# Kernel tuning notes

Hardware: AMD Instinct MI355X
Metric: run time of the kernel (lower is better)

The kernel has to match this reference:

```python
import jax, jax.numpy as jnp
import numpy as np

N, C_IN, C_OUT, H, RANK = 16, 4, 32, 400, 4


def setup_inputs() -> dict:
    key = jax.random.key(0)
    k1, k2, k3 = jax.random.split(key, 3)
    x = jax.random.normal(k1, (N, C_IN, H, H), dtype=jnp.float32)
    # symmetric sylo: weight_R tied to weight_L (shape C_out x C_in x H x rank)
    fan_in = C_IN * H
    scale = 1.0 / np.sqrt(fan_in)
    weight_L = jax.random.normal(k2, (C_OUT, C_IN, H, RANK), dtype=jnp.float32) * scale
    bias = jax.random.uniform(k3, (C_OUT,), dtype=jnp.float32, minval=-scale, maxval=scale)
    return {"x": x, "weight_L": weight_L, "bias": bias}


def reference(x, weight_L, bias):
    # Expand low-rank symmetric template: T[o,c] = L[o,c] @ L[o,c].T  (H x H)
    T = jnp.einsum('ocir,ocjr->ocij', weight_L, weight_L)
    # Crosshair similarity, summed over input channels:
    # out[n,o,i,j] = sum_c [ sum_k X[n,c,i,k]T[o,c,i,k] + sum_k X[n,c,k,j]T[o,c,k,j] - X[n,c,i,j]T[o,c,i,j] ]
    rows = jnp.einsum('ncik,ocik->noi', x, T)   # row sums of X*T
    cols = jnp.einsum('nckj,ockj->noj', x, T)   # column sums of X*T
    diag = jnp.einsum('ncij,ocij->noij', x, T)  # pointwise term (counted twice)
    out = rows[..., :, None] + cols[..., None, :] - diag
    return out + bias[None, :, None, None]
```

## Files before the change

kernel.cpp:

```cpp
#include <hip/hip_runtime.h>

#define H  400
#define NB 16
#define CI 4
#define CO 32

#define TT 80
__global__ __launch_bounds__(256) void k_transpose(const float* __restrict__ x,
                                                   float* __restrict__ xt) {
    __shared__ float tile[TT][TT + 5];
    int b = blockIdx.x;
    int tj = b % 5;
    int ti = (b / 5) % 5;
    int nc = b / 25;
    const float* src = x + (size_t)nc * H * H;
    float* dst = xt + (size_t)nc * H * H;
    int i0 = ti * TT, j0 = tj * TT;
    for (int e = threadIdx.x; e < TT * 20; e += 256) {
        int r = e / 20, q = e % 20;
        float4 v = ((const float4*)(src + (size_t)(i0 + r) * H + j0))[q];
        tile[r][q * 4 + 0] = v.x; tile[r][q * 4 + 1] = v.y;
        tile[r][q * 4 + 2] = v.z; tile[r][q * 4 + 3] = v.w;
    }
    __syncthreads();
    for (int e = threadIdx.x; e < TT * 20; e += 256) {
        int r = e / 20, q = e % 20;
        float4 v;
        v.x = tile[q * 4 + 0][r]; v.y = tile[q * 4 + 1][r];
        v.z = tile[q * 4 + 2][r]; v.w = tile[q * 4 + 3][r];
        ((float4*)(dst + (size_t)(j0 + r) * H + i0))[q] = v;
    }
}

#define KC 40
#define KSPLIT 5
__global__ __launch_bounds__(256) void k_rowscols(const float* __restrict__ x,
        const float* __restrict__ xt, const float* __restrict__ L,
        float* __restrict__ rowsP, float* __restrict__ colsP)
{
    __shared__ __align__(16) float4 Lm[CO * CI];
    __shared__ __align__(16) float Xr[NB * CI * KC];
    __shared__ __align__(16) float Xc[NB * CI * KC];
    __shared__ __align__(16) float Tr[CO * 164];
    int b = blockIdx.x;
    int m  = b / KSPLIT;
    int ks = b % KSPLIT;
    int tid = threadIdx.x;
    const float4* L4 = (const float4*)L;
    if (tid < CO * CI) Lm[tid] = L4[tid * H + m];

    int o  = tid & 31;
    int n0 = tid >> 5;
    int n1 = n0 + 8;
    float ar0 = 0.f, ar1 = 0.f, ac0 = 0.f, ac1 = 0.f;

    for (int ch = 0; ch < 2; ++ch) {
        int k0 = ks * 80 + ch * KC;
        __syncthreads();
        for (int e = tid; e < NB * CI * KC / 4; e += 256) {
            int q  = e % 10;
            int nc = e / 10;
            ((float4*)Xr)[e] = *(const float4*)(x  + (size_t)(nc * H + m) * H + k0 + q * 4);
            ((float4*)Xc)[e] = *(const float4*)(xt + (size_t)(nc * H + m) * H + k0 + q * 4);
        }
        for (int e = tid; e < CO * CI * KC; e += 256) {
            int k  = e % KC;
            int oc = e / KC;
            float4 lv = L4[oc * H + k0 + k];
            float4 lm = Lm[oc];
            Tr[(oc >> 2) * 164 + (oc & 3) * KC + k] =
                lv.x * lm.x + lv.y * lm.y + lv.z * lm.z + lv.w * lm.w;
        }
        __syncthreads();
        #pragma unroll
        for (int c = 0; c < CI; ++c) {
            const float4* trp = (const float4*)(Tr + o * 164 + c * KC);
            const float4* pr0 = (const float4*)(Xr + (n0 * CI + c) * KC);
            const float4* pr1 = (const float4*)(Xr + (n1 * CI + c) * KC);
            const float4* pc0 = (const float4*)(Xc + (n0 * CI + c) * KC);
            const float4* pc1 = (const float4*)(Xc + (n1 * CI + c) * KC);
            #pragma unroll
            for (int q = 0; q < KC / 4; ++q) {
                float4 tv = trp[q];
                float4 a  = pr0[q];
                float4 bb = pr1[q];
                float4 cc = pc0[q];
                float4 dd = pc1[q];
                ar0 += tv.x * a.x  + tv.y * a.y  + tv.z * a.z  + tv.w * a.w;
                ar1 += tv.x * bb.x + tv.y * bb.y + tv.z * bb.z + tv.w * bb.w;
                ac0 += tv.x * cc.x + tv.y * cc.y + tv.z * cc.z + tv.w * cc.w;
                ac1 += tv.x * dd.x + tv.y * dd.y + tv.z * dd.z + tv.w * dd.w;
            }
        }
    }
    size_t base = (size_t)ks * NB * CO * H;
    rowsP[base + (size_t)(n0 * CO + o) * H + m] = ar0;
    rowsP[base + (size_t)(n1 * CO + o) * H + m] = ar1;
    colsP[base + (size_t)(n0 * CO + o) * H + m] = ac0;
    colsP[base + (size_t)(n1 * CO + o) * H + m] = ac1;
}

__global__ __launch_bounds__(256) void k_reduce(const float* __restrict__ rowsP,
        const float* __restrict__ colsP, float* __restrict__ rows, float* __restrict__ cols)
{
    int i = blockIdx.x * 256 + threadIdx.x;
    if (i < NB * CO * H) {
        float s = 0.f, t = 0.f;
        #pragma unroll
        for (int k = 0; k < KSPLIT; ++k) {
            s += rowsP[(size_t)k * NB * CO * H + i];
            t += colsP[(size_t)k * NB * CO * H + i];
        }
        rows[i] = s;
        cols[i] = t;
    }
}

#define TS 16
__global__ __launch_bounds__(512) void k_out(const float* __restrict__ x,
        const float* __restrict__ L, const float* __restrict__ bias,
        const float* __restrict__ rows, const float* __restrict__ cols,
        float* __restrict__ out)
{
    __shared__ __align__(16) float Xl[NB * CI * TS * TS];
    __shared__ __align__(16) float rT[NB * 8 * TS];
    __shared__ __align__(16) float cT[NB * 8 * TS];
    int b = blockIdx.x;
    int ti = b / 25, tj = b % 25;
    int i0 = ti * TS, j0 = tj * TS;
    int tid = threadIdx.x;

    const float4* x4 = (const float4*)x;
    float4* Xl4 = (float4*)Xl;
    for (int e = tid; e < NB * CI * TS * 4; e += 512) {
        int q  = e & 3;
        int ii = (e >> 2) & 15;
        int nc = e >> 6;
        Xl4[e] = x4[(size_t)(nc * H + i0 + ii) * 100 + tj * 4 + q];
    }

    int o  = tid >> 6;
    int u  = tid & 63;
    int ii = u >> 2, jq = u & 3;
    const float4* L4 = (const float4*)L;
    const float4* cT4 = (const float4*)cT;
    float4* out4 = (float4*)out;

    for (int os = 0; os < 4; ++os) {
        int og = os * 8 + o;
        float4 T4[CI];
        #pragma unroll
        for (int c = 0; c < CI; ++c) {
            float4 Li = L4[(og * CI + c) * H + i0 + ii];
            float4 La = L4[(og * CI + c) * H + j0 + jq * 4 + 0];
            float4 Lb = L4[(og * CI + c) * H + j0 + jq * 4 + 1];
            float4 Lc = L4[(og * CI + c) * H + j0 + jq * 4 + 2];
            float4 Ld = L4[(og * CI + c) * H + j0 + jq * 4 + 3];
            T4[c].x = Li.x * La.x + Li.y * La.y + Li.z * La.z + Li.w * La.w;
            T4[c].y = Li.x * Lb.x + Li.y * Lb.y + Li.z * Lb.z + Li.w * Lb.w;
            T4[c].z = Li.x * Lc.x + Li.y * Lc.y + Li.z * Lc.z + Li.w * Lc.w;
            T4[c].w = Li.x * Ld.x + Li.y * Ld.y + Li.z * Ld.z + Li.w * Ld.w;
        }
        float bo = bias[og];

        __syncthreads();
        for (int e = tid; e < NB * 8 * TS; e += 512) {
            int iw = e & 15;
            int oo = (e >> 4) & 7;
            int n  = e >> 7;
            rT[e] = rows[(size_t)(n * CO + os * 8 + oo) * H + i0 + iw];
            cT[e] = cols[(size_t)(n * CO + os * 8 + oo) * H + j0 + iw];
        }
        __syncthreads();

        for (int n = 0; n < NB; ++n) {
            float ra = rT[(n * 8 + o) * TS + ii] + bo;
            float4 ca = cT4[(n * 8 + o) * 4 + jq];
            float4 acc;
            acc.x = ra + ca.x; acc.y = ra + ca.y; acc.z = ra + ca.z; acc.w = ra + ca.w;
            #pragma unroll
            for (int c = 0; c < CI; ++c) {
                float4 xv = Xl4[((n * CI + c) * TS + ii) * 4 + jq];
                acc.x -= xv.x * T4[c].x;
                acc.y -= xv.y * T4[c].y;
                acc.z -= xv.z * T4[c].z;
                acc.w -= xv.w * T4[c].w;
            }
            out4[((size_t)(n * CO + og) * H + i0 + ii) * 100 + tj * 4 + jq] = acc;
        }
    }
}

extern "C" void kernel_launch(void* const* d_in, const int* in_sizes, int n_in,
                              void* d_out, int out_size, void* d_ws, size_t ws_size,
                              hipStream_t stream) {
    const float* x    = (const float*)d_in[0];
    const float* L    = (const float*)d_in[1];
    const float* bias = (const float*)d_in[2];
    float* out = (float*)d_out;
    char* ws = (char*)d_ws;

    size_t xt_bytes = (size_t)NB * CI * H * H * sizeof(float);
    size_t rc_elems = (size_t)NB * CO * H;
    size_t rcP_bytes = (size_t)KSPLIT * rc_elems * sizeof(float);
    size_t rc_bytes  = rc_elems * sizeof(float);

    float* XT    = (float*)ws;
    float* rowsP = (float*)(ws + xt_bytes);
    float* colsP = (float*)(ws + xt_bytes + rcP_bytes);
    float* rows  = (float*)(ws + xt_bytes + 2 * rcP_bytes);
    float* cols  = (float*)(ws + xt_bytes + 2 * rcP_bytes + rc_bytes);
    (void)ws_size;

    k_transpose<<<1600, 256, 0, stream>>>(x, XT);
    k_rowscols<<<H * KSPLIT, 256, 0, stream>>>(x, XT, L, rowsP, colsP);
    k_reduce<<<(NB * CO * H + 255) / 256, 256, 0, stream>>>(rowsP, colsP, rows, cols);
    k_out<<<625, 512, 0, stream>>>(x, L, bias, rows, cols, out);
}
```

Measured before the change: 508.4 us.

## Shrink k_out blocks to 256 threads, split batch in halves; coalesce partial writes

k_out now runs 256-thread blocks that process the batch in two halves of 8 and loop over 8 output-channel groups of 4. This cuts shared memory per block so more blocks can be resident per CU, which should help latency hiding. k_rowscols now writes partial sums in an (ks, m, n*o) layout so each block's stores are contiguous, and k_reduce reads that layout and transposes back. In exchange, T is recomputed from L twice as often in k_out, there are more barriers, and k_reduce's reads become strided.

```diff
diff --git a/kernel.cpp b/kernel.cpp
--- a/kernel.cpp
+++ b/kernel.cpp
@@ -51,7 +51,6 @@
 
     int o  = tid & 31;
     int n0 = tid >> 5;
-    int n1 = n0 + 8;
     float ar0 = 0.f, ar1 = 0.f, ac0 = 0.f, ac1 = 0.f;
 
     for (int ch = 0; ch < 2; ++ch) {
@@ -76,9 +75,9 @@
         for (int c = 0; c < CI; ++c) {
             const float4* trp = (const float4*)(Tr + o * 164 + c * KC);
             const float4* pr0 = (const float4*)(Xr + (n0 * CI + c) * KC);
-            const float4* pr1 = (const float4*)(Xr + (n1 * CI + c) * KC);
+            const float4* pr1 = (const float4*)(Xr + ((n0 + 8) * CI + c) * KC);
             const float4* pc0 = (const float4*)(Xc + (n0 * CI + c) * KC);
-            const float4* pc1 = (const float4*)(Xc + (n1 * CI + c) * KC);
+            const float4* pc1 = (const float4*)(Xc + ((n0 + 8) * CI + c) * KC);
             #pragma unroll
             for (int q = 0; q < KC / 4; ++q) {
                 float4 tv = trp[q];
@@ -93,100 +92,104 @@
             }
         }
     }
-    size_t base = (size_t)ks * NB * CO * H;
-    rowsP[base + (size_t)(n0 * CO + o) * H + m] = ar0;
-    rowsP[base + (size_t)(n1 * CO + o) * H + m] = ar1;
-    colsP[base + (size_t)(n0 * CO + o) * H + m] = ac0;
-    colsP[base + (size_t)(n1 * CO + o) * H + m] = ac1;
+    size_t base = ((size_t)ks * H + m) * (NB * CO);
+    rowsP[base + tid]       = ar0;
+    rowsP[base + 256 + tid] = ar1;
+    colsP[base + tid]       = ac0;
+    colsP[base + 256 + tid] = ac1;
 }
 
 __global__ __launch_bounds__(256) void k_reduce(const float* __restrict__ rowsP,
         const float* __restrict__ colsP, float* __restrict__ rows, float* __restrict__ cols)
 {
     int i = blockIdx.x * 256 + threadIdx.x;
-    if (i < NB * CO * H) {
-        float s = 0.f, t = 0.f;
-        #pragma unroll
-        for (int k = 0; k < KSPLIT; ++k) {
-            s += rowsP[(size_t)k * NB * CO * H + i];
-            t += colsP[(size_t)k * NB * CO * H + i];
-        }
-        rows[i] = s;
-        cols[i] = t;
-    }
+    int m  = i % H;
+    int no = i / H;
+    float s = 0.f, t = 0.f;
+    #pragma unroll
+    for (int k = 0; k < KSPLIT; ++k) {
+        s += rowsP[((size_t)k * H + m) * (NB * CO) + no];
+        t += colsP[((size_t)k * H + m) * (NB * CO) + no];
+    }
+    rows[(size_t)no * H + m] = s;
+    cols[(size_t)no * H + m] = t;
 }
 
 #define TS 16
-__global__ __launch_bounds__(512) void k_out(const float* __restrict__ x,
+__global__ __launch_bounds__(256, 4) void k_out(const float* __restrict__ x,
         const float* __restrict__ L, const float* __restrict__ bias,
         const float* __restrict__ rows, const float* __restrict__ cols,
         float* __restrict__ out)
 {
-    __shared__ __align__(16) float Xl[NB * CI * TS * TS];
-    __shared__ __align__(16) float rT[NB * 8 * TS];
-    __shared__ __align__(16) float cT[NB * 8 * TS];
+    __shared__ __align__(16) float Xl[8 * CI * TS * TS];
+    __shared__ __align__(16) float rT[8 * 4 * TS];
+    __shared__ __align__(16) float cT[8 * 4 * TS];
     int b = blockIdx.x;
     int ti = b / 25, tj = b % 25;
     int i0 = ti * TS, j0 = tj * TS;
     int tid = threadIdx.x;
 
-    const float4* x4 = (const float4*)x;
-    float4* Xl4 = (float4*)Xl;
-    for (int e = tid; e < NB * CI * TS * 4; e += 512) {
-        int q  = e & 3;
-        int ii = (e >> 2) & 15;
-        int nc = e >> 6;
-        Xl4[e] = x4[(size_t)(nc * H + i0 + ii) * 100 + tj * 4 + q];
-    }
-
     int o  = tid >> 6;
     int u  = tid & 63;
     int ii = u >> 2, jq = u & 3;
-    const float4* L4 = (const float4*)L;
+    const float4* x4  = (const float4*)x;
+    const float4* L4  = (const float4*)L;
     const float4* cT4 = (const float4*)cT;
+    float4* Xl4  = (float4*)Xl;
     float4* out4 = (float4*)out;
 
-    for (int os = 0; os < 4; ++os) {
-        int og = os * 8 + o;
-        float4 T4[CI];
-        #pragma unroll
-        for (int c = 0; c < CI; ++c) {
-            float4 Li = L4[(og * CI + c) * H + i0 + ii];
-            float4 La = L4[(og * CI + c) * H + j0 + jq * 4 + 0];
-            float4 Lb = L4[(og * CI + c) * H + j0 + jq * 4 + 1];
-            float4 Lc = L4[(og * CI + c) * H + j0 + jq * 4 + 2];
-            float4 Ld = L4[(og * CI + c) * H + j0 + jq * 4 + 3];
-            T4[c].x = Li.x * La.x + Li.y * La.y + Li.z * La.z + Li.w * La.w;
-            T4[c].y = Li.x * Lb.x + Li.y * Lb.y + Li.z * Lb.z + Li.w * Lb.w;
-            T4[c].z = Li.x * Lc.x + Li.y * Lc.y + Li.z * Lc.z + Li.w * Lc.w;
-            T4[c].w = Li.x * Ld.x + Li.y * Ld.y + Li.z * Ld.z + Li.w * Ld.w;
-        }
-        float bo = bias[og];
-
-        __syncthreads();
-        for (int e = tid; e < NB * 8 * TS; e += 512) {
-            int iw = e & 15;
-            int oo = (e >> 4) & 7;
-            int n  = e >> 7;
-            rT[e] = rows[(size_t)(n * CO + os * 8 + oo) * H + i0 + iw];
-            cT[e] = cols[(size_t)(n * CO + os * 8 + oo) * H + j0 + iw];
-        }
-        __syncthreads();
-
-        for (int n = 0; n < NB; ++n) {
-            float ra = rT[(n * 8 + o) * TS + ii] + bo;
-            float4 ca = cT4[(n * 8 + o) * 4 + jq];
-            float4 acc;
-            acc.x = ra + ca.x; acc.y = ra + ca.y; acc.z = ra + ca.z; acc.w = ra + ca.w;
+    for (int nh = 0; nh < 2; ++nh) {
+        if (nh) __syncthreads();
+        for (int e = tid; e < 8 * CI * TS * 4; e += 256) {
+            int q   = e & 3;
+            int iiw = (e >> 2) & 15;
+            int nc  = nh * (8 * CI) + (e >> 6);
+            Xl4[e] = x4[(size_t)(nc * H + i0 + iiw) * 100 + tj * 4 + q];
+        }
+        for (int os = 0; os < 8; ++os) {
+            int og = os * 4 + o;
+            float4 T4[CI];
             #pragma unroll
             for (int c = 0; c < CI; ++c) {
-                float4 xv = Xl4[((n * CI + c) * TS + ii) * 4 + jq];
-                acc.x -= xv.x * T4[c].x;
-                acc.y -= xv.y * T4[c].y;
-                acc.z -= xv.z * T4[c].z;
-                acc.w -= xv.w * T4[c].w;
-            }
-            out4[((size_t)(n * CO + og) * H + i0 + ii) * 100 + tj * 4 + jq] = acc;
+                float4 Li = L4[(og * CI + c) * H + i0 + ii];
+                float4 La = L4[(og * CI + c) * H + j0 + jq * 4 + 0];
+                float4 Lb = L4[(og * CI + c) * H + j0 + jq * 4 + 1];
+                float4 Lc = L4[(og * CI + c) * H + j0 + jq * 4 + 2];
+                float4 Ld = L4[(og * CI + c) * H + j0 + jq * 4 + 3];
+                T4[c].x = Li.x * La.x + Li.y * La.y + Li.z * La.z + Li.w * La.w;
+                T4[c].y = Li.x * Lb.x + Li.y * Lb.y + Li.z * Lb.z + Li.w * Lb.w;
+                T4[c].z = Li.x * Lc.x + Li.y * Lc.y + Li.z * Lc.z + Li.w * Lc.w;
+                T4[c].w = Li.x * Ld.x + Li.y * Ld.y + Li.z * Ld.z + Li.w * Ld.w;
+            }
+            float bo = bias[og];
+
+            __syncthreads();
+            for (int e = tid; e < 8 * 4 * TS; e += 256) {
+                int iw = e & 15;
+                int oo = (e >> 4) & 3;
+                int np = e >> 6;
+                int n  = nh * 8 + np;
+                rT[e] = rows[(size_t)(n * CO + os * 4 + oo) * H + i0 + iw];
+                cT[e] = cols[(size_t)(n * CO + os * 4 + oo) * H + j0 + iw];
+            }
+            __syncthreads();
+
+            for (int np = 0; np < 8; ++np) {
+                float ra  = rT[(np * 4 + o) * TS + ii] + bo;
+                float4 ca = cT4[(np * 4 + o) * 4 + jq];
+                float4 acc;
+                acc.x = ra + ca.x; acc.y = ra + ca.y; acc.z = ra + ca.z; acc.w = ra + ca.w;
+                #pragma unroll
+                for (int c = 0; c < CI; ++c) {
+                    float4 xv = Xl4[((np * CI + c) * TS + ii) * 4 + jq];
+                    acc.x -= xv.x * T4[c].x;
+                    acc.y -= xv.y * T4[c].y;
+                    acc.z -= xv.z * T4[c].z;
+                    acc.w -= xv.w * T4[c].w;
+                }
+                int n = nh * 8 + np;
+                out4[((size_t)(n * CO + og) * H + i0 + ii) * 100 + tj * 4 + jq] = acc;
+            }
         }
     }
 }
@@ -214,6 +217,6 @@
 
     k_transpose<<<1600, 256, 0, stream>>>(x, XT);
     k_rowscols<<<H * KSPLIT, 256, 0, stream>>>(x, XT, L, rowsP, colsP);
-    k_reduce<<<(NB * CO * H + 255) / 256, 256, 0, stream>>>(rowsP, colsP, rows, cols);
-    k_out<<<625, 512, 0, stream>>>(x, L, bias, rows, cols, out);
-}
+    k_reduce<<<(NB * CO * H) / 256, 256, 0, stream>>>(rowsP, colsP, rows, cols);
+    k_out<<<625, 256, 0, stream>>>(x, L, bias, rows, cols, out);
+}
```

After: 504.0 us. About the same (-0.9%).
